# Optimization experiments

Measured on AMD Instinct MI355X. Metric: run time of the kernel, lower is better.

The kernel has to match this reference:

```python
import jax, jax.numpy as jnp
import numpy as np

D = 6
EPS = 1e-5


def layer_norm(x, w, b):
    m = jnp.mean(x, axis=-1, keepdims=True)
    v = jnp.mean(jnp.square(x - m), axis=-1, keepdims=True)
    return (x - m) * jax.lax.rsqrt(v + EPS) * w + b


def setup_inputs() -> dict:
    key = jax.random.key(0)
    ks = jax.random.split(key, 8)
    B, S = 8192, 128
    scale = 0.2
    return {
        "x": jax.random.normal(ks[0], (B, S, D), jnp.float32),
        "ln1_w": jnp.ones((D,), jnp.float32),
        "ln1_b": jnp.zeros((D,), jnp.float32),
        "wqkv": jax.random.normal(ks[1], (D, 3 * D), jnp.float32) * scale,
        "bqkv": jnp.zeros((3 * D,), jnp.float32),
        "wo": jax.random.normal(ks[2], (D, D), jnp.float32) * scale,
        "bo": jnp.zeros((D,), jnp.float32),
        "ln2_w": jnp.ones((D,), jnp.float32),
        "ln2_b": jnp.zeros((D,), jnp.float32),
        "w1": jax.random.normal(ks[3], (D, D), jnp.float32) * scale,
        "b1": jnp.zeros((D,), jnp.float32),
        "w2": jax.random.normal(ks[4], (D, D), jnp.float32) * scale,
        "b2": jnp.zeros((D,), jnp.float32),
    }


def reference(x, ln1_w, ln1_b, wqkv, bqkv, wo, bo, ln2_w, ln2_b, w1, b1, w2, b2):
    B, S, _ = x.shape
    # --- attention sub-block: x = x + attn(ln1(x)) ---
    h = layer_norm(x, ln1_w, ln1_b)                      # [B,S,D]
    qkv = h @ wqkv + bqkv                                # [B,S,3D]
    q, k, v = jnp.split(qkv, 3, axis=-1)
    scores = jnp.einsum('bqd,bkd->bqk', q, k) / jnp.sqrt(jnp.asarray(D, x.dtype))
    causal = jnp.tril(jnp.ones((S, S), bool))            # [S,S]
    scores = jnp.where(causal, scores, jnp.asarray(-1e9, x.dtype))
    attn = jax.nn.softmax(scores, axis=-1)               # [B,S,S]
    o = jnp.einsum('bqk,bkd->bqd', attn, v) @ wo + bo
    x = x + o
    # --- FFN sub-block: x = x + W2 @ gelu(W1 @ ln2(x)) ---
    h2 = layer_norm(x, ln2_w, ln2_b)
    ff = jax.nn.gelu(h2 @ w1 + b1, approximate=False) @ w2 + b2
    return x + ff
```

## Files before the change

kernel.cpp:

```cpp
#include <hip/hip_runtime.h>
#include <cmath>


typedef float    v2f  __attribute__((ext_vector_type(2)));
typedef float    f4v  __attribute__((ext_vector_type(4)));
typedef short    s4v  __attribute__((ext_vector_type(4)));
typedef uint32_t u2   __attribute__((ext_vector_type(2)));

constexpr int D = 6;
constexpr int S = 128;
#define EPS 1e-5f
#define RSQRT_D 0.4082482904638631f
#define LOG2E   1.4426950408889634f

#define EXP2F(x) __builtin_amdgcn_exp2f(x)
#define RCPF(x)  __builtin_amdgcn_rcpf(x)
#define PKFMA(a, b, c) __builtin_elementwise_fma((a), (b), (c))

union UA { uint32_t u[2]; u2 h; s4v v; };

__device__ __forceinline__ uint32_t pkbf(float hi, float lo) {
    return __builtin_amdgcn_perm(__builtin_bit_cast(uint32_t, hi),
                                 __builtin_bit_cast(uint32_t, lo),
                                 0x07060302u);
}
__device__ __forceinline__ uint16_t bf16t(float x) {
    return (uint16_t)(__builtin_bit_cast(uint32_t, x) >> 16);
}

__device__ __forceinline__ f4v mfma16(s4v a, s4v b, f4v c) {
#if __has_builtin(__builtin_amdgcn_mfma_f32_16x16x16bf16_1k)
    return __builtin_amdgcn_mfma_f32_16x16x16bf16_1k(a, b, c, 0, 0, 0);
#else
    f4v d;
    asm volatile("v_mfma_f32_16x16x16_bf16 %0, %1, %2, %3\n\t"
                 "s_nop 7\n\ts_nop 2"
                 : "=v"(d) : "v"(a), "v"(b), "v"(c));
    return d;
#endif
}

__global__ __launch_bounds__(S, 4) void txblock_kernel(
    const float* __restrict__ x,
    const float* __restrict__ ln1_w, const float* __restrict__ ln1_b,
    const float* __restrict__ wqkv,  const float* __restrict__ bqkv,
    const float* __restrict__ wo,    const float* __restrict__ bo,
    const float* __restrict__ ln2_w, const float* __restrict__ ln2_b,
    const float* __restrict__ w1,    const float* __restrict__ b1,
    const float* __restrict__ w2,    const float* __restrict__ b2,
    float* __restrict__ out)
{
    __shared__ uint32_t qlds[S][6];
    __shared__ uint32_t klds[S][6];
    __shared__ uint16_t vt[8][S + 8];
    __shared__ float    obuf[S][10];

    const int b = blockIdx.x;
    const int s = threadIdx.x;
    const float* xrow = x + ((size_t)b * S + s) * D;
    float*      orow = out + ((size_t)b * S + s) * D;

    v2f xv01 = ((const v2f*)xrow)[0];
    v2f xv23 = ((const v2f*)xrow)[1];
    v2f xv45 = ((const v2f*)xrow)[2];
    float xv[D] = {xv01[0], xv01[1], xv23[0], xv23[1], xv45[0], xv45[1]};

    float m = 0.f;
    #pragma unroll
    for (int d = 0; d < D; ++d) m += xv[d];
    m *= (1.0f / D);
    float var = 0.f;
    #pragma unroll
    for (int d = 0; d < D; ++d) { float t = xv[d] - m; var += t * t; }
    var *= (1.0f / D);
    float rstd = rsqrtf(var + EPS);
    float h1[D];
    #pragma unroll
    for (int d = 0; d < D; ++d)
        h1[d] = (xv[d] - m) * rstd * ln1_w[d] + ln1_b[d];

    v2f aq[3], ak[3], av[3];
    #pragma unroll
    for (int jp = 0; jp < 3; ++jp) {
        aq[jp] = ((const v2f*)bqkv)[jp];
        ak[jp] = ((const v2f*)(bqkv + D))[jp];
        av[jp] = ((const v2f*)(bqkv + 2 * D))[jp];
    }
    #pragma unroll
    for (int d = 0; d < D; ++d) {
        const float* wrow = wqkv + d * 3 * D;
        v2f hd = {h1[d], h1[d]};
        #pragma unroll
        for (int jp = 0; jp < 3; ++jp) {
            aq[jp] = PKFMA(hd, ((const v2f*)wrow)[jp], aq[jp]);
            ak[jp] = PKFMA(hd, ((const v2f*)(wrow + D))[jp], ak[jp]);
            av[jp] = PKFMA(hd, ((const v2f*)(wrow + 2 * D))[jp], av[jp]);
        }
    }
    const v2f qscale = {RSQRT_D * LOG2E, RSQRT_D * LOG2E};

    #pragma unroll
    for (int jp = 0; jp < 3; ++jp) {
        v2f qs = aq[jp] * qscale;
        qlds[s][jp] = pkbf(qs[1], qs[0]);
        klds[s][jp] = pkbf(ak[jp][1], ak[jp][0]);
    }
    qlds[s][3] = 0; qlds[s][4] = 0; qlds[s][5] = 0;
    klds[s][3] = 0; klds[s][4] = 0; klds[s][5] = 0;
    vt[0][s] = bf16t(av[0][0]);
    vt[1][s] = bf16t(av[0][1]);
    vt[2][s] = bf16t(av[1][0]);
    vt[3][s] = bf16t(av[1][1]);
    vt[4][s] = bf16t(av[2][0]);
    vt[5][s] = bf16t(av[2][1]);
    vt[6][s] = 0x3F80;
    vt[7][s] = 0;
    __syncthreads();

    const int wv  = s >> 6;
    const int l15 = s & 15;
    const int lq  = (s >> 4) & 3;
    const int aoff = (lq < 2) ? lq * 8 : 16;
    const int vne  = (l15 < 7) ? l15 : 7;

    #pragma unroll
    for (int i = 0; i < 4; ++i) {
        static const int QT0[4] = {0, 3, 4, 7};
        static const int QT1[4] = {1, 2, 5, 6};
        const int qt = wv ? QT1[i] : QT0[i];
        UA qf; qf.h = *(const u2*)((const char*)&qlds[qt * 16 + l15][0] + aoff);
        f4v O = {0.f, 0.f, 0.f, 0.f};
        for (int jt = 0; jt <= qt; ++jt) {
            UA kf; kf.h = *(const u2*)((const char*)&klds[jt * 16 + l15][0] + aoff);
            f4v c = mfma16(kf.v, qf.v, (f4v){0.f, 0.f, 0.f, 0.f});
            float p0 = EXP2F(c[0]);
            float p1 = EXP2F(c[1]);
            float p2 = EXP2F(c[2]);
            float p3 = EXP2F(c[3]);
            if (jt == qt) {
                p0 = (lq * 4 + 0 > l15) ? 0.f : p0;
                p1 = (lq * 4 + 1 > l15) ? 0.f : p1;
                p2 = (lq * 4 + 2 > l15) ? 0.f : p2;
                p3 = (lq * 4 + 3 > l15) ? 0.f : p3;
            }
            UA pa;
            pa.u[0] = pkbf(p1, p0);
            pa.u[1] = pkbf(p3, p2);
            UA vf; vf.h = *(const u2*)&vt[vne][jt * 16 + lq * 4];
            O = mfma16(pa.v, vf.v, O);
        }
        if (l15 < 7) {
            #pragma unroll
            for (int r = 0; r < 4; ++r)
                obuf[qt * 16 + lq * 4 + r][l15] = O[r];
        }
    }
    __syncthreads();

    v2f o01 = *(const v2f*)&obuf[s][0];
    v2f o23 = *(const v2f*)&obuf[s][2];
    v2f o45 = *(const v2f*)&obuf[s][4];
    float invl = RCPF(obuf[s][6]);
    v2f il = {invl, invl};
    o01 *= il; o23 *= il; o45 *= il;
    float av6[D] = {o01[0], o01[1], o23[0], o23[1], o45[0], o45[1]};

    v2f xvp[3] = {xv01, xv23, xv45};
    v2f x2p[3];
    #pragma unroll
    for (int dp = 0; dp < 3; ++dp) {
        v2f o = ((const v2f*)bo)[dp];
        #pragma unroll
        for (int e = 0; e < D; ++e) {
            v2f we = ((const v2f*)(wo + e * D))[dp];
            v2f ae = {av6[e], av6[e]};
            o = PKFMA(ae, we, o);
        }
        x2p[dp] = o + xvp[dp];
    }
    float x2[D] = {x2p[0][0], x2p[0][1], x2p[1][0], x2p[1][1], x2p[2][0], x2p[2][1]};

    float m2 = 0.f;
    #pragma unroll
    for (int d = 0; d < D; ++d) m2 += x2[d];
    m2 *= (1.0f / D);
    float var2 = 0.f;
    #pragma unroll
    for (int d = 0; d < D; ++d) { float t = x2[d] - m2; var2 += t * t; }
    var2 *= (1.0f / D);
    float rstd2 = rsqrtf(var2 + EPS);
    float h2[D];
    #pragma unroll
    for (int d = 0; d < D; ++d)
        h2[d] = (x2[d] - m2) * rstd2 * ln2_w[d] + ln2_b[d];

    v2f ap[3];
    #pragma unroll
    for (int jp = 0; jp < 3; ++jp) {
        v2f a = ((const v2f*)b1)[jp];
        #pragma unroll
        for (int d = 0; d < D; ++d) {
            v2f wd = ((const v2f*)(w1 + d * D))[jp];
            v2f hd = {h2[d], h2[d]};
            a = PKFMA(hd, wd, a);
        }
        ap[jp] = a;
    }
    float g[D];
    #pragma unroll
    for (int j = 0; j < D; ++j) {
        float a = ap[j >> 1][j & 1];
        float t  = a * a;
        float in = fmaf(0.044715f * t, a, a);
        float e  = EXP2F(in * -2.3022229f);
        float r  = RCPF(1.0f + e);
        g[j] = a * r;
    }
    #pragma unroll
    for (int dp = 0; dp < 3; ++dp) {
        v2f a = ((const v2f*)b2)[dp];
        #pragma unroll
        for (int e = 0; e < D; ++e) {
            v2f we = ((const v2f*)(w2 + e * D))[dp];
            v2f ge = {g[e], g[e]};
            a = PKFMA(ge, we, a);
        }
        ((v2f*)orow)[dp] = x2p[dp] + a;
    }
}

extern "C" void kernel_launch(void* const* d_in, const int* in_sizes, int n_in,
                              void* d_out, int out_size, void* d_ws, size_t ws_size,
                              hipStream_t stream) {
    const float* x     = (const float*)d_in[0];
    const float* ln1_w = (const float*)d_in[1];
    const float* ln1_b = (const float*)d_in[2];
    const float* wqkv  = (const float*)d_in[3];
    const float* bqkv  = (const float*)d_in[4];
    const float* wo    = (const float*)d_in[5];
    const float* bo    = (const float*)d_in[6];
    const float* ln2_w = (const float*)d_in[7];
    const float* ln2_b = (const float*)d_in[8];
    const float* w1    = (const float*)d_in[9];
    const float* b1    = (const float*)d_in[10];
    const float* w2    = (const float*)d_in[11];
    const float* b2    = (const float*)d_in[12];
    float* out = (float*)d_out;

    const int B = in_sizes[0] / (S * D);
    txblock_kernel<<<B, S, 0, stream>>>(x, ln1_w, ln1_b, wqkv, bqkv, wo, bo,
                                        ln2_w, ln2_b, w1, b1, w2, b2, out);
}
```

Baseline: 116.6 us.

## Preload K/V fragments into registers and interleave paired query tiles

Loads all eight K and V MFMA fragments from LDS into registers once per wave instead of reloading them for every query tile. Processes query tiles in compile-time pairs (0/7, 3/4, 1/6, 2/5) with fully unrolled inner loops, interleaving the two independent MFMA/exp chains to hide MFMA latency. This cuts repeated LDS reads and loop overhead but raises register pressure and code size.

```diff
diff --git a/kernel.cpp b/kernel.cpp
--- a/kernel.cpp
+++ b/kernel.cpp
@@ -38,6 +38,62 @@
                  : "=v"(d) : "v"(a), "v"(b), "v"(c));
     return d;
 #endif
+}
+
+template<int QA, int QB>
+__device__ __forceinline__ void attn_pair(
+    const UA (&kf)[8], const UA (&vf)[8],
+    const uint32_t (*qlds)[6], float (*obuf)[10],
+    int l15, int lq, int aoff)
+{
+    UA qfA, qfB;
+    qfA.h = *(const u2*)((const char*)&qlds[QA * 16 + l15][0] + aoff);
+    qfB.h = *(const u2*)((const char*)&qlds[QB * 16 + l15][0] + aoff);
+    const f4v z = {0.f, 0.f, 0.f, 0.f};
+    f4v OA = z, OB = z;
+    #pragma unroll
+    for (int jt = 0; jt <= QB; ++jt) {
+        f4v cB = mfma16(kf[jt].v, qfB.v, z);
+        f4v cA;
+        if (jt <= QA) cA = mfma16(kf[jt].v, qfA.v, z);
+        float pB0 = EXP2F(cB[0]);
+        float pB1 = EXP2F(cB[1]);
+        float pB2 = EXP2F(cB[2]);
+        float pB3 = EXP2F(cB[3]);
+        if (jt == QB) {
+            pB0 = (lq * 4 + 0 > l15) ? 0.f : pB0;
+            pB1 = (lq * 4 + 1 > l15) ? 0.f : pB1;
+            pB2 = (lq * 4 + 2 > l15) ? 0.f : pB2;
+            pB3 = (lq * 4 + 3 > l15) ? 0.f : pB3;
+        }
+        UA paB;
+        paB.u[0] = pkbf(pB1, pB0);
+        paB.u[1] = pkbf(pB3, pB2);
+        OB = mfma16(paB.v, vf[jt].v, OB);
+        if (jt <= QA) {
+            float pA0 = EXP2F(cA[0]);
+            float pA1 = EXP2F(cA[1]);
+            float pA2 = EXP2F(cA[2]);
+            float pA3 = EXP2F(cA[3]);
+            if (jt == QA) {
+                pA0 = (lq * 4 + 0 > l15) ? 0.f : pA0;
+                pA1 = (lq * 4 + 1 > l15) ? 0.f : pA1;
+                pA2 = (lq * 4 + 2 > l15) ? 0.f : pA2;
+                pA3 = (lq * 4 + 3 > l15) ? 0.f : pA3;
+            }
+            UA paA;
+            paA.u[0] = pkbf(pA1, pA0);
+            paA.u[1] = pkbf(pA3, pA2);
+            OA = mfma16(paA.v, vf[jt].v, OA);
+        }
+    }
+    if (l15 < 7) {
+        #pragma unroll
+        for (int r = 0; r < 4; ++r) {
+            obuf[QA * 16 + lq * 4 + r][l15] = OA[r];
+            obuf[QB * 16 + lq * 4 + r][l15] = OB[r];
+        }
+    }
 }
 
 __global__ __launch_bounds__(S, 4) void txblock_kernel(
@@ -123,37 +179,19 @@
     const int aoff = (lq < 2) ? lq * 8 : 16;
     const int vne  = (l15 < 7) ? l15 : 7;
 
-    #pragma unroll
-    for (int i = 0; i < 4; ++i) {
-        static const int QT0[4] = {0, 3, 4, 7};
-        static const int QT1[4] = {1, 2, 5, 6};
-        const int qt = wv ? QT1[i] : QT0[i];
-        UA qf; qf.h = *(const u2*)((const char*)&qlds[qt * 16 + l15][0] + aoff);
-        f4v O = {0.f, 0.f, 0.f, 0.f};
-        for (int jt = 0; jt <= qt; ++jt) {
-            UA kf; kf.h = *(const u2*)((const char*)&klds[jt * 16 + l15][0] + aoff);
-            f4v c = mfma16(kf.v, qf.v, (f4v){0.f, 0.f, 0.f, 0.f});
-            float p0 = EXP2F(c[0]);
-            float p1 = EXP2F(c[1]);
-            float p2 = EXP2F(c[2]);
-            float p3 = EXP2F(c[3]);
-            if (jt == qt) {
-                p0 = (lq * 4 + 0 > l15) ? 0.f : p0;
-                p1 = (lq * 4 + 1 > l15) ? 0.f : p1;
-                p2 = (lq * 4 + 2 > l15) ? 0.f : p2;
-                p3 = (lq * 4 + 3 > l15) ? 0.f : p3;
-            }
-            UA pa;
-            pa.u[0] = pkbf(p1, p0);
-            pa.u[1] = pkbf(p3, p2);
-            UA vf; vf.h = *(const u2*)&vt[vne][jt * 16 + lq * 4];
-            O = mfma16(pa.v, vf.v, O);
-        }
-        if (l15 < 7) {
-            #pragma unroll
-            for (int r = 0; r < 4; ++r)
-                obuf[qt * 16 + lq * 4 + r][l15] = O[r];
-        }
+    UA kf[8], vf[8];
+    #pragma unroll
+    for (int jt = 0; jt < 8; ++jt) {
+        kf[jt].h = *(const u2*)((const char*)&klds[jt * 16 + l15][0] + aoff);
+        vf[jt].h = *(const u2*)&vt[vne][jt * 16 + lq * 4];
+    }
+
+    if (wv == 0) {
+        attn_pair<0, 7>(kf, vf, qlds, obuf, l15, lq, aoff);
+        attn_pair<3, 4>(kf, vf, qlds, obuf, l15, lq, aoff);
+    } else {
+        attn_pair<1, 6>(kf, vf, qlds, obuf, l15, lq, aoff);
+        attn_pair<2, 5>(kf, vf, qlds, obuf, l15, lq, aoff);
     }
     __syncthreads();
 
```

Result: faster. 112.5 us (-3.5%).

## Interleave four query tiles per wave and redistribute attention output via shuffles

Applied to the files above, without the earlier changes.

Restructures the attention loop so each wave processes its four query tiles together, sharing K/V fragment loads across them. The PV MFMA operands are swapped so output lands transposed, and results are redistributed with cross-lane shuffles instead of an LDS buffer plus a second barrier. Each thread then handles a different row and reloads x from global memory for it. Launch bounds are raised to 8 blocks per CU, which adds register pressure from four live accumulators.

```diff
diff --git a/kernel.cpp b/kernel.cpp
--- a/kernel.cpp
+++ b/kernel.cpp
@@ -40,7 +40,74 @@
 #endif
 }
 
-__global__ __launch_bounds__(S, 4) void txblock_kernel(
+__device__ __forceinline__ void stream_step(
+    const UA& kf, const UA& vf, const UA& qf, f4v& O,
+    bool diag, int l15, int lq)
+{
+    const f4v z = {0.f, 0.f, 0.f, 0.f};
+    f4v c = mfma16(kf.v, qf.v, z);
+    float p0 = EXP2F(c[0]);
+    float p1 = EXP2F(c[1]);
+    float p2 = EXP2F(c[2]);
+    float p3 = EXP2F(c[3]);
+    if (diag) {
+        p0 = (lq * 4 + 0 > l15) ? 0.f : p0;
+        p1 = (lq * 4 + 1 > l15) ? 0.f : p1;
+        p2 = (lq * 4 + 2 > l15) ? 0.f : p2;
+        p3 = (lq * 4 + 3 > l15) ? 0.f : p3;
+    }
+    UA pa;
+    pa.u[0] = pkbf(p1, p0);
+    pa.u[1] = pkbf(p3, p2);
+    O = mfma16(vf.v, pa.v, O);
+}
+
+template<int T0, int T1, int T2, int T3>
+__device__ __forceinline__ int attn_quad(
+    const uint32_t (*qlds)[6], const uint32_t (*klds)[6],
+    const uint16_t (*vt)[S + 8],
+    int l15, int lq, int aoff, int vne,
+    float& d0, float& d1, float& d2, float& d3,
+    float& d4, float& d5, float& dl)
+{
+    UA q0, q1, q2, q3;
+    q0.h = *(const u2*)((const char*)&qlds[T0 * 16 + l15][0] + aoff);
+    q1.h = *(const u2*)((const char*)&qlds[T1 * 16 + l15][0] + aoff);
+    q2.h = *(const u2*)((const char*)&qlds[T2 * 16 + l15][0] + aoff);
+    q3.h = *(const u2*)((const char*)&qlds[T3 * 16 + l15][0] + aoff);
+    const f4v z = {0.f, 0.f, 0.f, 0.f};
+    f4v O0 = z, O1 = z, O2 = z, O3 = z;
+    #pragma unroll
+    for (int jt = 0; jt <= T3; ++jt) {
+        UA kf; kf.h = *(const u2*)((const char*)&klds[jt * 16 + l15][0] + aoff);
+        UA vf; vf.h = *(const u2*)&vt[vne][jt * 16 + lq * 4];
+        if (jt <= T0) stream_step(kf, vf, q0, O0, jt == T0, l15, lq);
+        if (jt <= T1) stream_step(kf, vf, q1, O1, jt == T1, l15, lq);
+        if (jt <= T2) stream_step(kf, vf, q2, O2, jt == T2, l15, lq);
+        stream_step(kf, vf, q3, O3, jt == T3, l15, lq);
+    }
+    const int lqx = lq ^ 1;
+    float selfC[4], sendC[4], otherC[4];
+    #pragma unroll
+    for (int r = 0; r < 4; ++r) {
+        selfC[r] = (lq  == 0) ? O0[r] : (lq  == 1) ? O1[r] : (lq  == 2) ? O2[r] : O3[r];
+        sendC[r] = (lqx == 0) ? O0[r] : (lqx == 1) ? O1[r] : (lqx == 2) ? O2[r] : O3[r];
+    }
+    #pragma unroll
+    for (int r = 0; r < 4; ++r) otherC[r] = __shfl_xor(sendC[r], 16);
+    const bool lp = ((lq & 1) == 0);
+    d0 = lp ? selfC[0] : otherC[0];
+    d1 = lp ? selfC[1] : otherC[1];
+    d2 = lp ? selfC[2] : otherC[2];
+    d3 = lp ? selfC[3] : otherC[3];
+    d4 = lp ? otherC[0] : selfC[0];
+    d5 = lp ? otherC[1] : selfC[1];
+    dl = lp ? otherC[2] : selfC[2];
+    const int myT = (lq == 0) ? T0 : (lq == 1) ? T1 : (lq == 2) ? T2 : T3;
+    return myT * 16 + l15;
+}
+
+__global__ __launch_bounds__(S, 8) void txblock_kernel(
     const float* __restrict__ x,
     const float* __restrict__ ln1_w, const float* __restrict__ ln1_b,
     const float* __restrict__ wqkv,  const float* __restrict__ bqkv,
@@ -53,12 +120,10 @@
     __shared__ uint32_t qlds[S][6];
     __shared__ uint32_t klds[S][6];
     __shared__ uint16_t vt[8][S + 8];
-    __shared__ float    obuf[S][10];
 
     const int b = blockIdx.x;
     const int s = threadIdx.x;
     const float* xrow = x + ((size_t)b * S + s) * D;
-    float*      orow = out + ((size_t)b * S + s) * D;
 
     v2f xv01 = ((const v2f*)xrow)[0];
     v2f xv23 = ((const v2f*)xrow)[1];
@@ -121,51 +186,27 @@
     const int l15 = s & 15;
     const int lq  = (s >> 4) & 3;
     const int aoff = (lq < 2) ? lq * 8 : 16;
-    const int vne  = (l15 < 7) ? l15 : 7;
-
-    #pragma unroll
-    for (int i = 0; i < 4; ++i) {
-        static const int QT0[4] = {0, 3, 4, 7};
-        static const int QT1[4] = {1, 2, 5, 6};
-        const int qt = wv ? QT1[i] : QT0[i];
-        UA qf; qf.h = *(const u2*)((const char*)&qlds[qt * 16 + l15][0] + aoff);
-        f4v O = {0.f, 0.f, 0.f, 0.f};
-        for (int jt = 0; jt <= qt; ++jt) {
-            UA kf; kf.h = *(const u2*)((const char*)&klds[jt * 16 + l15][0] + aoff);
-            f4v c = mfma16(kf.v, qf.v, (f4v){0.f, 0.f, 0.f, 0.f});
-            float p0 = EXP2F(c[0]);
-            float p1 = EXP2F(c[1]);
-            float p2 = EXP2F(c[2]);
-            float p3 = EXP2F(c[3]);
-            if (jt == qt) {
-                p0 = (lq * 4 + 0 > l15) ? 0.f : p0;
-                p1 = (lq * 4 + 1 > l15) ? 0.f : p1;
-                p2 = (lq * 4 + 2 > l15) ? 0.f : p2;
-                p3 = (lq * 4 + 3 > l15) ? 0.f : p3;
-            }
-            UA pa;
-            pa.u[0] = pkbf(p1, p0);
-            pa.u[1] = pkbf(p3, p2);
-            UA vf; vf.h = *(const u2*)&vt[vne][jt * 16 + lq * 4];
-            O = mfma16(pa.v, vf.v, O);
-        }
-        if (l15 < 7) {
-            #pragma unroll
-            for (int r = 0; r < 4; ++r)
-                obuf[qt * 16 + lq * 4 + r][l15] = O[r];
-        }
-    }
-    __syncthreads();
-
-    v2f o01 = *(const v2f*)&obuf[s][0];
-    v2f o23 = *(const v2f*)&obuf[s][2];
-    v2f o45 = *(const v2f*)&obuf[s][4];
-    float invl = RCPF(obuf[s][6]);
-    v2f il = {invl, invl};
-    o01 *= il; o23 *= il; o45 *= il;
-    float av6[D] = {o01[0], o01[1], o23[0], o23[1], o45[0], o45[1]};
-
-    v2f xvp[3] = {xv01, xv23, xv45};
+    const int vne  = l15 & 7;
+
+    float d0, d1, d2, d3, d4, d5, dl;
+    int row;
+    if (wv == 0)
+        row = attn_quad<0, 3, 4, 7>(qlds, klds, vt, l15, lq, aoff, vne,
+                                    d0, d1, d2, d3, d4, d5, dl);
+    else
+        row = attn_quad<1, 2, 5, 6>(qlds, klds, vt, l15, lq, aoff, vne,
+                                    d0, d1, d2, d3, d4, d5, dl);
+
+    float invl = RCPF(dl);
+    float av6[D] = {d0 * invl, d1 * invl, d2 * invl,
+                    d3 * invl, d4 * invl, d5 * invl};
+
+    const float* xr = x + ((size_t)b * S + row) * D;
+    v2f rx01 = ((const v2f*)xr)[0];
+    v2f rx23 = ((const v2f*)xr)[1];
+    v2f rx45 = ((const v2f*)xr)[2];
+
+    v2f xvp[3] = {rx01, rx23, rx45};
     v2f x2p[3];
     #pragma unroll
     for (int dp = 0; dp < 3; ++dp) {
@@ -216,6 +257,7 @@
         float r  = RCPF(1.0f + e);
         g[j] = a * r;
     }
+    float* orow = out + ((size_t)b * S + row) * D;
     #pragma unroll
     for (int dp = 0; dp < 3; ++dp) {
         v2f a = ((const v2f*)b2)[dp];
```

New measurement: 115.9 us. Within noise of the previous version (-0.6%).
